# Kernel optimization log

Hardware: AMD Instinct MI355X
Metric: run time of the kernel (lower is better)

The kernel has to match this reference:

```python
import jax, jax.numpy as jnp
import numpy as np
from jax import lax

N, L, V, ES, HS = 16384, 512, 32000, 32, 64


def setup_inputs() -> dict:
    key = jax.random.key(0)
    k_tok, k_len, k_emb, k_wih, k_whh, k_bih, k_bhh = jax.random.split(key, 7)
    # valid tokens in [1, V) so that (x != 0).sum(1) == true prefix length
    tok = jax.random.randint(k_tok, (N, L), 1, V)
    lengths = jax.random.randint(k_len, (N,), 0, L + 1)  # includes empty seqs
    x = jnp.where(jnp.arange(L)[None, :] < lengths[:, None], tok, 0)
    s = 0.1
    embedding = jax.random.normal(k_emb, (V, ES), dtype=jnp.float32) * s
    w_ih = jax.random.normal(k_wih, (3 * HS, ES), dtype=jnp.float32) * s  # [r|z|n] stacked (torch order)
    w_hh = jax.random.normal(k_whh, (3 * HS, HS), dtype=jnp.float32) * s
    b_ih = jax.random.normal(k_bih, (3 * HS,), dtype=jnp.float32) * s
    b_hh = jax.random.normal(k_bhh, (3 * HS,), dtype=jnp.float32) * s
    return {"x": x, "embedding": embedding, "w_ih": w_ih, "w_hh": w_hh,
            "b_ih": b_ih, "b_hh": b_hh}


def reference(x, embedding, w_ih, w_hh, b_ih, b_hh):
    # Faithful math: final GRU hidden state over the nonzero prefix of each row;
    # rows with length 0 return zeros (h0). Equivalent to bucketed
    # pack_padded_sequence + GRU + scatter of final hidden states.
    n, l = x.shape
    hs = w_hh.shape[1]
    lengths = (x != 0).sum(axis=1)  # [n]

    def step(h, inp):
        t, xt = inp                      # xt: [n] token ids at time t
        e = embedding[xt]                # [n, es] gather
        gx = e @ w_ih.T + b_ih           # [n, 3*hs]
        gh = h @ w_hh.T + b_hh           # [n, 3*hs]
        xr, xz, xn = jnp.split(gx, 3, axis=-1)
        hr, hz, hn = jnp.split(gh, 3, axis=-1)
        r = jax.nn.sigmoid(xr + hr)
        z = jax.nn.sigmoid(xz + hz)
        ng = jnp.tanh(xn + r * hn)
        h_new = (1.0 - z) * ng + z * h   # torch GRU update
        h = jnp.where((t < lengths)[:, None], h_new, h)  # freeze past length
        return h, None

    h0 = jnp.zeros((n, hs), dtype=embedding.dtype)
    hT, _ = lax.scan(step, h0, (jnp.arange(l), x.T))
    return hT
```

## Files before the change

### kernel.cpp

```cpp
#include <hip/hip_runtime.h>

#define N_SEQ 16384
#define LSEQ  512
#define VOCAB 32000
#define ES    32
#define HS    64
#define LDH   72
#define TS    18

#define SC_RZ (-1.4426950408889634f)
#define SC_N  (-2.8853900817779268f)

typedef _Float16 v8h __attribute__((ext_vector_type(8)));
typedef float    v4f __attribute__((ext_vector_type(4)));

#define NLB (N_SEQ / 4)
#define NEB (VOCAB * ES / 2048)
__global__ __launch_bounds__(256) void k_prep(const int* __restrict__ x,
                                              const float* __restrict__ emb,
                                              const float* __restrict__ whh,
                                              const float* __restrict__ wih,
                                              int* __restrict__ len,
                                              int* __restrict__ hist,
                                              _Float16* __restrict__ ef,
                                              _Float16* __restrict__ wpk,
                                              _Float16* __restrict__ wpe){
  int b = blockIdx.x;
  if (b < NLB){
    int row  = b * 4 + (threadIdx.x >> 6);
    int lane = threadIdx.x & 63;
    const int4* xr = (const int4*)(x + (size_t)row * LSEQ);
    int cnt = 0;
    #pragma unroll
    for (int i = 0; i < 2; ++i){
      int4 v = xr[lane + i*64];
      cnt += (v.x != 0) + (v.y != 0) + (v.z != 0) + (v.w != 0);
    }
    #pragma unroll
    for (int d = 1; d < 64; d <<= 1) cnt += __shfl_xor(cnt, d, 64);
    if (lane == 0){ len[row] = cnt; atomicAdd(&hist[cnt], 1); }
  } else if (b < NLB + NEB){
    int i = ((b - NLB) * 256 + threadIdx.x) * 8;
    float4 f0 = *(const float4*)(emb + i);
    float4 f1 = *(const float4*)(emb + i + 4);
    v8h o;
    o[0] = (_Float16)f0.x; o[1] = (_Float16)f0.y;
    o[2] = (_Float16)f0.z; o[3] = (_Float16)f0.w;
    o[4] = (_Float16)f1.x; o[5] = (_Float16)f1.y;
    o[6] = (_Float16)f1.z; o[7] = (_Float16)f1.w;
    *(v8h*)(ef + i) = o;
  } else {
    int tid = (b - NLB - NEB) * 256 + threadIdx.x;
    if (tid < 1536){
      int f = tid >> 6, l = tid & 63;
      int jt = f >> 1, kf = f & 1;
      float sc = (jt < 8) ? SC_RZ : SC_N;
      #pragma unroll
      for (int i = 0; i < 8; ++i){
        int row = jt * 16 + (l & 15);
        int col = kf * 32 + (l >> 4) * 8 + i;
        wpk[(size_t)tid * 8 + i] = (_Float16)(sc * whh[row * HS + col]);
      }
    } else if (tid < 1536 + 768){
      int t2 = tid - 1536;
      int tile = t2 >> 6, l = t2 & 63;
      float sc = ((tile >> 2) < 2) ? SC_RZ : SC_N;
      #pragma unroll
      for (int i = 0; i < 8; ++i){
        int row = tile * 16 + (l & 15);
        int col = (l >> 4) * 8 + i;
        wpe[(size_t)t2 * 8 + i] = (_Float16)(sc * wih[row * ES + col]);
      }
    }
  }
}

__global__ __launch_bounds__(1024) void k_scatter(const int* __restrict__ hist,
                                                  const int* __restrict__ len,
                                                  int* __restrict__ gcnt,
                                                  int* __restrict__ perm){
  __shared__ int buf[1024];
  __shared__ int offs[513];
  int i = threadIdx.x;
  buf[i] = (i < 513) ? hist[i] : 0;
  __syncthreads();
  for (int d = 1; d < 1024; d <<= 1){
    int v = (i >= d) ? buf[i - d] : 0;
    __syncthreads();
    buf[i] += v;
    __syncthreads();
  }
  if (i < 513) offs[i] = (i == 0) ? 0 : buf[i - 1];
  __syncthreads();
  int s = blockIdx.x * 1024 + i;
  int l = len[s];
  int pos = offs[l] + atomicAdd(&gcnt[l], 1);
  perm[pos] = s;
}

__global__ __launch_bounds__(256, 4) void k_gru(
    const int* __restrict__ x, const _Float16* __restrict__ ef,
    const _Float16* __restrict__ wpk, const _Float16* __restrict__ wpe,
    const float* __restrict__ bih, const float* __restrict__ bhh,
    const int* __restrict__ perm, const int* __restrict__ len,
    float* __restrict__ out)
{
  __shared__ __align__(16) _Float16 hb[2][16 * LDH];
  __shared__ unsigned short tok[(LSEQ + 2) * TS];
  int qt   = threadIdx.x >> 6;
  int w = blockIdx.x >> 8, cq = blockIdx.x & 255;
  int rank = w * 256 + ((w & 1) ? (255 - cq) : cq);
  int grp  = 1023 - rank;
  int lane = threadIdx.x & 63;
  int q = lane >> 4, c = lane & 15;
  int uu = qt*16 + c;

  v8h bfh[3][2], bfe[3];
  #pragma unroll
  for (int g = 0; g < 3; ++g){
    int tile = g*4 + qt;
    #pragma unroll
    for (int kf = 0; kf < 2; ++kf)
      bfh[g][kf] = *(const v8h*)(wpk + ((size_t)(tile*2 + kf)*64 + lane)*8);
    bfe[g] = *(const v8h*)(wpe + ((size_t)tile*64 + lane)*8);
  }

  int sq[4], ln[4];
  #pragma unroll
  for (int r = 0; r < 4; ++r){
    int s = perm[grp * 16 + q*4 + r];
    sq[r] = s;
    ln[r] = len[s];
  }
  float br  = SC_RZ * (bih[uu]      + bhh[uu]);
  float bz  = SC_RZ * (bih[HS + uu] + bhh[HS + uu]);
  float ben = SC_N  *  bih[2*HS + uu];
  float bhn = SC_N  *  bhh[2*HS + uu];
  v4f brq  = {br, br, br, br};
  v4f bzq  = {bz, bz, bz, bz};
  v4f benq = {ben, ben, ben, ben};
  v4f bhnq = {bhn, bhn, bhn, bhn};
  const v4f zero4 = {0.f, 0.f, 0.f, 0.f};

  float h[4];
  #pragma unroll
  for (int r = 0; r < 4; ++r) h[r] = 0.f;

  for (int i = threadIdx.x; i < 16*LDH; i += 256) hb[0][i] = (_Float16)0.f;

  for (int j = threadIdx.x; j < 16*LSEQ; j += 256){
    int s = j >> 9, tt = j & (LSEQ-1);
    tok[tt*TS + s] = (unsigned short)x[(size_t)perm[grp*16 + s] * LSEQ + tt];
  }
  if (threadIdx.x < 32){
    tok[(LSEQ + (threadIdx.x >> 4))*TS + (threadIdx.x & 15)] = 0;
  }
  __syncthreads();

  int tmax = max(max(ln[0], ln[1]), max(ln[2], ln[3]));
  tmax = max(tmax, __shfl_xor(tmax, 16, 64));
  tmax = max(tmax, __shfl_xor(tmax, 32, 64));
  int tmin = min(min(ln[0], ln[1]), min(ln[2], ln[3]));
  tmin = min(tmin, __shfl_xor(tmin, 16, 64));
  tmin = min(tmin, __shfl_xor(tmin, 32, 64));

  v8h aec, aen;
  v4f pra, prb, pza, pzb, dea, deb;
  {
    int tk0 = tok[0*TS + c];
    aec = *(const v8h*)(ef + (size_t)tk0 * ES + q*8);
    pra = __builtin_amdgcn_mfma_f32_16x16x32_f16(aec, bfe[0], brq,  0,0,0);
    pza = __builtin_amdgcn_mfma_f32_16x16x32_f16(aec, bfe[1], bzq,  0,0,0);
    dea = __builtin_amdgcn_mfma_f32_16x16x32_f16(aec, bfe[2], benq, 0,0,0);
    int tk1 = tok[1*TS + c];
    aen = *(const v8h*)(ef + (size_t)tk1 * ES + q*8);
  }

  #define GRU_STEP(FREEZE, ACONS, ALOAD, PRR, PRZ, DEN, PRRn, PRZn, DENn, RB, WB) \
  {                                                                            \
    int tkn = tok[(t + 2)*TS + c];                                             \
    v8h a0 = *(const v8h*)(&hb[RB][c*LDH + q*8]);                              \
    v8h a1 = *(const v8h*)(&hb[RB][c*LDH + 32 + q*8]);                         \
    v4f ur  = __builtin_amdgcn_mfma_f32_16x16x32_f16(a1, bfh[0][1], PRR, 0,0,0);\
    v4f vr  = __builtin_amdgcn_mfma_f32_16x16x32_f16(a0, bfh[0][0], zero4,0,0,0);\
    v4f uz  = __builtin_amdgcn_mfma_f32_16x16x32_f16(a1, bfh[1][1], PRZ, 0,0,0);\
    v4f vz  = __builtin_amdgcn_mfma_f32_16x16x32_f16(a0, bfh[1][0], zero4,0,0,0);\
    v4f uh  = __builtin_amdgcn_mfma_f32_16x16x32_f16(a1, bfh[2][1], bhnq,0,0,0);\
    v4f vh  = __builtin_amdgcn_mfma_f32_16x16x32_f16(a0, bfh[2][0], zero4,0,0,0);\
    v4f Dr  = ur + vr;                                                         \
    v4f Dz  = uz + vz;                                                         \
    v4f Dhn = uh + vh;                                                         \
    _Pragma("unroll")                                                          \
    for (int r = 0; r < 4; ++r){                                               \
      float rg   = __builtin_amdgcn_rcpf(1.f + __builtin_amdgcn_exp2f(Dr[r])); \
      float zg   = __builtin_amdgcn_rcpf(1.f + __builtin_amdgcn_exp2f(Dz[r])); \
      float te   = __builtin_amdgcn_exp2f(DEN[r] + rg * Dhn[r]);               \
      float ng   = fmaf(2.f, __builtin_amdgcn_rcpf(1.f + te), -1.f);           \
      float hnew = ng + zg * (h[r] - ng);                                      \
      h[r]       = (FREEZE && t >= ln[r]) ? h[r] : hnew;                       \
    }                                                                          \
    _Pragma("unroll")                                                          \
    for (int r = 0; r < 4; ++r)                                                \
      hb[WB][(q*4 + r)*LDH + uu] = (_Float16)h[r];                             \
    PRRn = __builtin_amdgcn_mfma_f32_16x16x32_f16(ACONS, bfe[0], brq,  0,0,0); \
    PRZn = __builtin_amdgcn_mfma_f32_16x16x32_f16(ACONS, bfe[1], bzq,  0,0,0); \
    DENn = __builtin_amdgcn_mfma_f32_16x16x32_f16(ACONS, bfe[2], benq, 0,0,0); \
    ALOAD = *(const v8h*)(ef + (size_t)tkn * ES + q*8);           \
    asm volatile("s_waitcnt lgkmcnt(0)" ::: "memory");                         \
    __builtin_amdgcn_s_barrier();                                              \
    asm volatile("" ::: "memory");                                             \
  }

  int t = 0;
  for (; t + 1 < tmin; ){
    GRU_STEP(0, aen, aec, pra, pza, dea, prb, pzb, deb, 0, 1); ++t;
    GRU_STEP(0, aec, aen, prb, pzb, deb, pra, pza, dea, 1, 0); ++t;
  }
  for (; t + 1 < tmax; ){
    GRU_STEP(1, aen, aec, pra, pza, dea, prb, pzb, deb, 0, 1); ++t;
    GRU_STEP(1, aec, aen, prb, pzb, deb, pra, pza, dea, 1, 0); ++t;
  }
  if (t < tmax){
    GRU_STEP(1, aen, aec, pra, pza, dea, prb, pzb, deb, 0, 1); ++t;
  }
  #undef GRU_STEP

  #pragma unroll
  for (int r = 0; r < 4; ++r)
    out[(size_t)sq[r] * HS + uu] = h[r];
}

extern "C" void kernel_launch(void* const* d_in, const int* in_sizes, int n_in,
                              void* d_out, int out_size, void* d_ws, size_t ws_size,
                              hipStream_t stream){
  const int*   x   = (const int*)  d_in[0];
  const float* emb = (const float*)d_in[1];
  const float* wih = (const float*)d_in[2];
  const float* whh = (const float*)d_in[3];
  const float* bih = (const float*)d_in[4];
  const float* bhh = (const float*)d_in[5];
  float* out = (float*)d_out;

  char* ws = (char*)d_ws;
  size_t off = 0;
  _Float16* ef  = (_Float16*)(ws + off);  off += (size_t)VOCAB * ES * sizeof(_Float16);
  _Float16* wpk = (_Float16*)(ws + off);  off += (size_t)24 * 64 * 8 * sizeof(_Float16);
  _Float16* wpe = (_Float16*)(ws + off);  off += (size_t)12 * 64 * 8 * sizeof(_Float16);
  off = (off + 255) & ~(size_t)255;
  int* len  = (int*)(ws + off);           off += (size_t)N_SEQ * sizeof(int);
  int* perm = (int*)(ws + off);           off += (size_t)N_SEQ * sizeof(int);
  int* hist = (int*)(ws + off);           off += 513 * sizeof(int);
  int* gcnt = (int*)(ws + off);           off += 513 * sizeof(int);

  hipMemsetAsync(hist, 0, 2 * 513 * sizeof(int), stream);
  k_prep   <<<NLB + NEB + 9, 256, 0, stream>>>(x, emb, whh, wih, len, hist, ef, wpk, wpe);
  k_scatter<<<N_SEQ / 1024, 1024, 0, stream>>>(hist, len, gcnt, perm);
  k_gru    <<<N_SEQ / 16,    256, 0, stream>>>(x, ef, wpk, wpe, bih, bhh, perm, len, out);
}
```

Measured before the change: 322.5 us.

## Drop memset and global histogram; chain MFMA accumulation with priority hints

Removes the hipMemsetAsync and the global atomic histogram: k_prep now zeroes gcnt in an extra block, and each k_scatter block rebuilds the length histogram in shared memory from len. In the GRU step, the two half-K MFMAs per gate are chained through the accumulator instead of being summed with separate vector adds, and the MFMA groups are wrapped in s_setprio. The input-projection MFMAs and embedding load are moved ahead of the hidden-state LDS writes. The chained MFMAs add a dependency that may lengthen the serial critical path, and every scatter block now recomputes the full histogram.

```diff
diff --git a/kernel.cpp b/kernel.cpp
--- a/kernel.cpp
+++ b/kernel.cpp
@@ -21,7 +21,7 @@
                                               const float* __restrict__ whh,
                                               const float* __restrict__ wih,
                                               int* __restrict__ len,
-                                              int* __restrict__ hist,
+                                              int* __restrict__ gcnt,
                                               _Float16* __restrict__ ef,
                                               _Float16* __restrict__ wpk,
                                               _Float16* __restrict__ wpe){
@@ -38,7 +38,7 @@
     }
     #pragma unroll
     for (int d = 1; d < 64; d <<= 1) cnt += __shfl_xor(cnt, d, 64);
-    if (lane == 0){ len[row] = cnt; atomicAdd(&hist[cnt], 1); }
+    if (lane == 0) len[row] = cnt;
   } else if (b < NLB + NEB){
     int i = ((b - NLB) * 256 + threadIdx.x) * 8;
     float4 f0 = *(const float4*)(emb + i);
@@ -49,40 +49,43 @@
     o[4] = (_Float16)f1.x; o[5] = (_Float16)f1.y;
     o[6] = (_Float16)f1.z; o[7] = (_Float16)f1.w;
     *(v8h*)(ef + i) = o;
+  } else if (b < NLB + NEB + 6){
+    int tid = (b - NLB - NEB) * 256 + threadIdx.x;
+    int f = tid >> 6, l = tid & 63;
+    int jt = f >> 1, kf = f & 1;
+    float sc = (jt < 8) ? SC_RZ : SC_N;
+    #pragma unroll
+    for (int i = 0; i < 8; ++i){
+      int row = jt * 16 + (l & 15);
+      int col = kf * 32 + (l >> 4) * 8 + i;
+      wpk[(size_t)tid * 8 + i] = (_Float16)(sc * whh[row * HS + col]);
+    }
+  } else if (b < NLB + NEB + 9){
+    int t2 = (b - NLB - NEB - 6) * 256 + threadIdx.x;
+    int tile = t2 >> 6, l = t2 & 63;
+    float sc = ((tile >> 2) < 2) ? SC_RZ : SC_N;
+    #pragma unroll
+    for (int i = 0; i < 8; ++i){
+      int row = tile * 16 + (l & 15);
+      int col = (l >> 4) * 8 + i;
+      wpe[(size_t)t2 * 8 + i] = (_Float16)(sc * wih[row * ES + col]);
+    }
   } else {
-    int tid = (b - NLB - NEB) * 256 + threadIdx.x;
-    if (tid < 1536){
-      int f = tid >> 6, l = tid & 63;
-      int jt = f >> 1, kf = f & 1;
-      float sc = (jt < 8) ? SC_RZ : SC_N;
-      #pragma unroll
-      for (int i = 0; i < 8; ++i){
-        int row = jt * 16 + (l & 15);
-        int col = kf * 32 + (l >> 4) * 8 + i;
-        wpk[(size_t)tid * 8 + i] = (_Float16)(sc * whh[row * HS + col]);
-      }
-    } else if (tid < 1536 + 768){
-      int t2 = tid - 1536;
-      int tile = t2 >> 6, l = t2 & 63;
-      float sc = ((tile >> 2) < 2) ? SC_RZ : SC_N;
-      #pragma unroll
-      for (int i = 0; i < 8; ++i){
-        int row = tile * 16 + (l & 15);
-        int col = (l >> 4) * 8 + i;
-        wpe[(size_t)t2 * 8 + i] = (_Float16)(sc * wih[row * ES + col]);
-      }
-    }
-  }
-}
-
-__global__ __launch_bounds__(1024) void k_scatter(const int* __restrict__ hist,
-                                                  const int* __restrict__ len,
+    for (int i = threadIdx.x; i < 513; i += 256) gcnt[i] = 0;
+  }
+}
+
+__global__ __launch_bounds__(1024) void k_scatter(const int* __restrict__ len,
                                                   int* __restrict__ gcnt,
                                                   int* __restrict__ perm){
   __shared__ int buf[1024];
   __shared__ int offs[513];
   int i = threadIdx.x;
-  buf[i] = (i < 513) ? hist[i] : 0;
+  buf[i] = 0;
+  __syncthreads();
+  #pragma unroll
+  for (int k = 0; k < 16; ++k)
+    atomicAdd(&buf[len[k * 1024 + i]], 1);
   __syncthreads();
   for (int d = 1; d < 1024; d <<= 1){
     int v = (i >= d) ? buf[i - d] : 0;
@@ -140,7 +143,6 @@
   v4f bzq  = {bz, bz, bz, bz};
   v4f benq = {ben, ben, ben, ben};
   v4f bhnq = {bhn, bhn, bhn, bhn};
-  const v4f zero4 = {0.f, 0.f, 0.f, 0.f};
 
   float h[4];
   #pragma unroll
@@ -181,15 +183,14 @@
     int tkn = tok[(t + 2)*TS + c];                                             \
     v8h a0 = *(const v8h*)(&hb[RB][c*LDH + q*8]);                              \
     v8h a1 = *(const v8h*)(&hb[RB][c*LDH + 32 + q*8]);                         \
-    v4f ur  = __builtin_amdgcn_mfma_f32_16x16x32_f16(a1, bfh[0][1], PRR, 0,0,0);\
-    v4f vr  = __builtin_amdgcn_mfma_f32_16x16x32_f16(a0, bfh[0][0], zero4,0,0,0);\
-    v4f uz  = __builtin_amdgcn_mfma_f32_16x16x32_f16(a1, bfh[1][1], PRZ, 0,0,0);\
-    v4f vz  = __builtin_amdgcn_mfma_f32_16x16x32_f16(a0, bfh[1][0], zero4,0,0,0);\
-    v4f uh  = __builtin_amdgcn_mfma_f32_16x16x32_f16(a1, bfh[2][1], bhnq,0,0,0);\
-    v4f vh  = __builtin_amdgcn_mfma_f32_16x16x32_f16(a0, bfh[2][0], zero4,0,0,0);\
-    v4f Dr  = ur + vr;                                                         \
-    v4f Dz  = uz + vz;                                                         \
-    v4f Dhn = uh + vh;                                                         \
+    __builtin_amdgcn_s_setprio(1);                                             \
+    v4f zr  = __builtin_amdgcn_mfma_f32_16x16x32_f16(a1, bfh[0][1], PRR, 0,0,0);\
+    v4f Dr  = __builtin_amdgcn_mfma_f32_16x16x32_f16(a0, bfh[0][0], zr,  0,0,0);\
+    v4f zz  = __builtin_amdgcn_mfma_f32_16x16x32_f16(a1, bfh[1][1], PRZ, 0,0,0);\
+    v4f Dz  = __builtin_amdgcn_mfma_f32_16x16x32_f16(a0, bfh[1][0], zz,  0,0,0);\
+    v4f zh  = __builtin_amdgcn_mfma_f32_16x16x32_f16(a1, bfh[2][1], bhnq,0,0,0);\
+    v4f Dhn = __builtin_amdgcn_mfma_f32_16x16x32_f16(a0, bfh[2][0], zh,  0,0,0);\
+    __builtin_amdgcn_s_setprio(0);                                             \
     _Pragma("unroll")                                                          \
     for (int r = 0; r < 4; ++r){                                               \
       float rg   = __builtin_amdgcn_rcpf(1.f + __builtin_amdgcn_exp2f(Dr[r])); \
@@ -199,13 +200,15 @@
       float hnew = ng + zg * (h[r] - ng);                                      \
       h[r]       = (FREEZE && t >= ln[r]) ? h[r] : hnew;                       \
     }                                                                          \
+    __builtin_amdgcn_s_setprio(1);                                             \
+    PRRn = __builtin_amdgcn_mfma_f32_16x16x32_f16(ACONS, bfe[0], brq,  0,0,0); \
+    PRZn = __builtin_amdgcn_mfma_f32_16x16x32_f16(ACONS, bfe[1], bzq,  0,0,0); \
+    DENn = __builtin_amdgcn_mfma_f32_16x16x32_f16(ACONS, bfe[2], benq, 0,0,0); \
+    __builtin_amdgcn_s_setprio(0);                                             \
+    ALOAD = *(const v8h*)(ef + (size_t)tkn * ES + q*8);           \
     _Pragma("unroll")                                                          \
     for (int r = 0; r < 4; ++r)                                                \
       hb[WB][(q*4 + r)*LDH + uu] = (_Float16)h[r];                             \
-    PRRn = __builtin_amdgcn_mfma_f32_16x16x32_f16(ACONS, bfe[0], brq,  0,0,0); \
-    PRZn = __builtin_amdgcn_mfma_f32_16x16x32_f16(ACONS, bfe[1], bzq,  0,0,0); \
-    DENn = __builtin_amdgcn_mfma_f32_16x16x32_f16(ACONS, bfe[2], benq, 0,0,0); \
-    ALOAD = *(const v8h*)(ef + (size_t)tkn * ES + q*8);           \
     asm volatile("s_waitcnt lgkmcnt(0)" ::: "memory");                         \
     __builtin_amdgcn_s_barrier();                                              \
     asm volatile("" ::: "memory");                                             \
@@ -249,11 +252,9 @@
   off = (off + 255) & ~(size_t)255;
   int* len  = (int*)(ws + off);           off += (size_t)N_SEQ * sizeof(int);
   int* perm = (int*)(ws + off);           off += (size_t)N_SEQ * sizeof(int);
-  int* hist = (int*)(ws + off);           off += 513 * sizeof(int);
   int* gcnt = (int*)(ws + off);           off += 513 * sizeof(int);
 
-  hipMemsetAsync(hist, 0, 2 * 513 * sizeof(int), stream);
-  k_prep   <<<NLB + NEB + 9, 256, 0, stream>>>(x, emb, whh, wih, len, hist, ef, wpk, wpe);
-  k_scatter<<<N_SEQ / 1024, 1024, 0, stream>>>(hist, len, gcnt, perm);
+  k_prep   <<<NLB + NEB + 10, 256, 0, stream>>>(x, emb, whh, wih, len, gcnt, ef, wpk, wpe);
+  k_scatter<<<N_SEQ / 1024, 1024, 0, stream>>>(len, gcnt, perm);
   k_gru    <<<N_SEQ / 16,    256, 0, stream>>>(x, ef, wpk, wpe, bih, bhh, perm, len, out);
 }
```

Result: faster. 299.1 us (-7.2%).
